# Optimization experiments

Measured on AMD Instinct MI355X. Metric: run time of the kernel, lower is better.

The kernel has to match this reference:

```python
import jax, jax.numpy as jnp
import numpy as np
import math

B, S_TOK = 2, 2046
NC = 2
S = S_TOK + NC                 # 2048 total sequence after prepending condition tokens
D, D_INNER, V = 512, 2048, 512
L, H, MAX_SEQ = 6, 8, 2048
DH = D // H
PAD = 0


def setup_inputs() -> dict:
    key = jax.random.key(0)
    ks = iter(jax.random.split(key, 48))
    def nrm(shape, scale=0.02):
        return jax.random.normal(next(ks), shape, jnp.float32) * scale
    inp = {}
    inp["x_tokens"] = jax.random.randint(next(ks), (B, S_TOK), 0, V)
    inp["conditions"] = jax.random.normal(next(ks), (B, NC), jnp.float32)
    inp["times_to_chord"] = jax.random.uniform(next(ks), (B, S_TOK), jnp.float32) * 8.0
    inp["emb"] = nrm((V, D), 0.1).at[PAD].set(0.0)  # padding_idx row zeroed
    inp["pos"] = nrm((1, MAX_SEQ, D), 0.1)
    inp["cond_W1"] = nrm((NC, 1, D // 2)); inp["cond_b1"] = jnp.zeros((NC, D // 2))
    inp["cond_W2"] = nrm((NC, D // 2, D)); inp["cond_b2"] = jnp.zeros((NC, D))
    inp["null_cond"] = nrm((NC, D), 0.1)
    inp["ttc_W"] = nrm((1, D_INNER)); inp["ttc_b"] = jnp.zeros((D_INNER,))
    for nm in ["Wq", "Wk", "Wv", "Wo"]:
        inp[nm] = nrm((L, D, D))
    for nm in ["bq", "bk", "bv", "bo"]:
        inp[nm] = jnp.zeros((L, D))
    inp["E"] = nrm((L, MAX_SEQ, DH), 1.0)  # torch.randn relative-position embedding
    inp["ffn_W1"] = nrm((L, D, D_INNER)); inp["ffn_b1"] = jnp.zeros((L, D_INNER))
    inp["ffn_W2"] = nrm((L, D_INNER, D)); inp["ffn_b2"] = jnp.zeros((L, D))
    inp["ln1_g"] = jnp.ones((L, D)); inp["ln1_b"] = jnp.zeros((L, D))
    inp["ln2_g"] = jnp.ones((L, D)); inp["ln2_b"] = jnp.zeros((L, D))
    inp["fc_W"] = nrm((D, V), 0.1); inp["fc_b"] = jnp.zeros((V,))
    return inp


def _layer_norm(x, g, b, eps=1e-6):
    mu = x.mean(-1, keepdims=True)
    var = ((x - mu) ** 2).mean(-1, keepdims=True)
    return (x - mu) / jnp.sqrt(var + eps) * g + b


def _rel_attn(x, bias, Wq, bq, Wk, bk, Wv, bv, Wo, bo, E):
    # RelativeGlobalAttention: QE masking + skewing trick (Huang et al. 2018)
    Bb, Sq, _ = x.shape
    q = (x @ Wq + bq).reshape(Bb, Sq, H, DH).transpose(0, 2, 1, 3)  # [B,H,S,dh]
    k = (x @ Wk + bk).reshape(Bb, Sq, H, DH).transpose(0, 2, 1, 3)
    v = (x @ Wv + bv).reshape(Bb, Sq, H, DH).transpose(0, 2, 1, 3)
    e = E[MAX_SEQ - Sq:]                                  # [M,dh], M == Sq here
    QE = jnp.einsum('bhld,md->bhlm', q, e)                # [B,H,S,M]
    M = QE.shape[-1]
    # row l keeps columns m >= M-1-l  (torch _qe_masking)
    qe_mask = (jnp.arange(M)[None, :] >= (M - 1 - jnp.arange(Sq))[:, None])
    QE = QE * qe_mask.astype(QE.dtype)
    # skewing: pad one column on the left, reshape, drop first row
    padded = jnp.pad(QE, ((0, 0), (0, 0), (0, 0), (1, 0)))
    Srel = padded.reshape(Bb, H, M + 1, Sq)[:, :, 1:, :]  # [B,H,S,S]
    logits = (jnp.einsum('bhld,bhmd->bhlm', q, k) + Srel) / math.sqrt(DH) + bias
    attn = jax.nn.softmax(logits, axis=-1)
    out = jnp.einsum('bhlm,bhmd->bhld', attn, v)
    out = out.transpose(0, 2, 1, 3).reshape(Bb, Sq, D)
    return out @ Wo + bo


def _forward(x_tokens, conditions, times_to_chord, emb, pos, cond_W1, cond_b1,
             cond_W2, cond_b2, null_cond, ttc_W, ttc_b, Wq, bq, Wk, bk, Wv, bv,
             Wo, bo, E, ffn_W1, ffn_b1, ffn_W2, ffn_b2, ln1_g, ln1_b, ln2_g,
             ln2_b, fc_W, fc_b):
    x = emb[x_tokens] * math.sqrt(D)                      # [B,S_tok,D]
    # generate_mask on tokens padded with -1 for the NC condition slots
    tok_pad = jnp.pad(x_tokens, ((0, 0), (NC, 0)), constant_values=-1)
    causal = jnp.triu(jnp.ones((S, S), bool), 1)          # True above diagonal
    key_pad = tok_pad == PAD                              # [B,S] pad keys
    attn_bias = jnp.where(causal[None] | key_pad[:, None, :],
                          -jnp.inf, 0.0)[:, None]         # [B,1,S,S]
    # condition MLPs with NaN -> learned null-condition substitution
    c = conditions[..., None]                             # [B,NC,1]
    nan = jnp.isnan(c)
    cm = jnp.where(nan, 0.0, c)
    h1 = jax.nn.relu(jnp.einsum('bci,cio->bco', cm, cond_W1) + cond_b1[None])
    ce = jnp.einsum('bci,cio->bco', h1, cond_W2) + cond_b2[None]   # [B,NC,D]
    ce = jnp.where(nan, null_cond[None], ce)
    x = jnp.concatenate([ce, x], axis=1)                  # [B,S,D]
    ttc = jnp.concatenate([jnp.repeat(times_to_chord[:, :1], NC, axis=1),
                           times_to_chord], axis=1)       # [B,S]
    chord = (8.0 - ttc)[..., None] @ ttc_W + ttc_b        # [B,S,D_INNER]
    x = x + pos[:, :S]
    for l in range(L):
        attn_out = _rel_attn(x, attn_bias, Wq[l], bq[l], Wk[l], bk[l],
                             Wv[l], bv[l], Wo[l], bo[l], E[l])
        out1 = _layer_norm(attn_out + x, ln1_g[l], ln1_b[l])
        ffn = jax.nn.relu(out1 @ ffn_W1[l] + ffn_b1[l]) + chord
        ffn = ffn @ ffn_W2[l] + ffn_b2[l]
        x = _layer_norm(out1 + ffn, ln2_g[l], ln2_b[l])
    return x @ fc_W + fc_b                                # [B,S,V]


def reference(x_tokens, conditions, times_to_chord, emb, pos, cond_W1, cond_b1,
              cond_W2, cond_b2, null_cond, ttc_W, ttc_b, Wq, bq, Wk, bk, Wv, bv,
              Wo, bo, E, ffn_W1, ffn_b1, ffn_W2, ffn_b2, ln1_g, ln1_b, ln2_g,
              ln2_b, fc_W, fc_b):
    return _forward(x_tokens, conditions, times_to_chord, emb, pos, cond_W1,
                    cond_b1, cond_W2, cond_b2, null_cond, ttc_W, ttc_b, Wq, bq,
                    Wk, bk, Wv, bv, Wo, bo, E, ffn_W1, ffn_b1, ffn_W2, ffn_b2,
                    ln1_g, ln1_b, ln2_g, ln2_b, fc_W, fc_b)
```

## Files before the change

kernel.cpp:

```cpp
#include <hip/hip_runtime.h>
#include <hip/hip_bf16.h>
#include <math.h>

#define BATCH  2
#define S_TOK  2046
#define NCOND  2
#define SEQ    2048
#define DMODEL 512
#define DINNER 2048
#define NHEAD  8
#define DHEAD  64
#define NLAYER 6
#define VOCAB  512
#define MROWS  (BATCH*SEQ)

#define NSLOT_G 144
#define NSLOTS  (16 * NSLOT_G)

typedef unsigned short bf16u;
typedef __attribute__((ext_vector_type(8))) short s8frag;
typedef __attribute__((ext_vector_type(4))) float f4frag;

__device__ __forceinline__ float b2f(bf16u u) {
  union { unsigned int i; float f; } v; v.i = ((unsigned int)u) << 16; return v.f;
}
__device__ __forceinline__ bf16u f2b(float f) {
  union { float f; unsigned int i; } v; v.f = f;
  unsigned int x = v.i;
  return (bf16u)((x + 0x7fffu + ((x >> 16) & 1u)) >> 16);
}
__device__ __forceinline__ unsigned int pack2(float a, float b) {
  return (unsigned int)f2b(a) | ((unsigned int)f2b(b) << 16);
}

__device__ __forceinline__ void gld16(const bf16u* g, bf16u* l) {
  __builtin_amdgcn_global_load_lds(
      (const __attribute__((address_space(1))) unsigned int*)g,
      (__attribute__((address_space(3))) unsigned int*)l,
      16, 0, 0);
}

#define DPP_ROR(dst, src, N)                                              \
  dst = __int_as_float(__builtin_amdgcn_update_dpp(                       \
      0, __float_as_int(src), 0x120 + (N), 0xF, 0xF, true))

__device__ __forceinline__ int slot_off(int it) {
  int a = it >> 2, b = it & 3;
  return it + 2 * a * (a - 1) + a * b;
}

__global__ __launch_bounds__(256) void wt_all_kernel(
    const float* __restrict__ Wq, const float* __restrict__ Wk,
    const float* __restrict__ Wv, const float* __restrict__ Wo,
    const float* __restrict__ W1, const float* __restrict__ W2,
    const float* __restrict__ fcW,
    bf16u* __restrict__ qkvT, bf16u* __restrict__ oT,
    bf16u* __restrict__ w1T, bf16u* __restrict__ w2T, bf16u* __restrict__ fcT)
{
  int bid = blockIdx.x;
  const float* src; bf16u* dst; int N, K, kt, nt;
  if (bid < 6 * 768) {
    int L = bid / 768, t = bid - L * 768;
    if (t < 256) {
      int mat = t >> 6, tt = t & 63;
      const float* s4[4] = {Wq, Wk, Wv, Wo};
      src = s4[mat] + (size_t)L * DMODEL * DMODEL;
      dst = (mat < 3) ? (qkvT + (size_t)L * 786432 + (size_t)mat * 262144)
                      : (oT + (size_t)L * 262144);
      K = DMODEL; N = DMODEL; kt = tt >> 3; nt = tt & 7;
    } else if (t < 512) {
      int tt = t - 256;
      src = W1 + (size_t)L * DMODEL * DINNER; dst = w1T + (size_t)L * 1048576;
      K = DMODEL; N = DINNER; kt = tt >> 5; nt = tt & 31;
    } else {
      int tt = t - 512;
      src = W2 + (size_t)L * DINNER * DMODEL; dst = w2T + (size_t)L * 1048576;
      K = DINNER; N = DMODEL; kt = tt >> 3; nt = tt & 7;
    }
  } else {
    int tt = bid - 6 * 768;
    src = fcW; dst = fcT;
    K = DMODEL; N = VOCAB; kt = tt >> 3; nt = tt & 7;
  }
  __shared__ bf16u Ls[64][66];
  int tid = threadIdx.x;
  int c = tid & 63, r4 = tid >> 6;
#pragma unroll
  for (int i = 0; i < 16; i++) {
    int r = i * 4 + r4;
    Ls[r][c] = f2b(src[(size_t)(kt * 64 + r) * N + nt * 64 + c]);
  }
  __syncthreads();
#pragma unroll
  for (int i = 0; i < 16; i++) {
    int rr = i * 4 + r4;
    dst[(size_t)(nt * 64 + rr) * K + kt * 64 + c] = Ls[c][rr];
  }
}

template <int RB>
__global__ __launch_bounds__(256) void mgemm(
    const bf16u* __restrict__ A, const bf16u* __restrict__ Wt,
    const float* __restrict__ b0, const float* __restrict__ b1,
    const float* __restrict__ b2, const bf16u* __restrict__ Rb,
    float* __restrict__ Cf, bf16u* __restrict__ Cb,
    int M, int N, int K, int mode,
    const float* __restrict__ ttc, const float* __restrict__ ttcW,
    const float* __restrict__ ttcb)
{
  __shared__ bf16u Ab[RB * 32][64];
  __shared__ bf16u Bb[128][64];
  const int tid = threadIdx.x;
  const int lane = tid & 63, wave = tid >> 6;
  const int quad = lane >> 4, l16 = lane & 15;
  const int wm = wave >> 1, wn = wave & 1;

  const int nwg = gridDim.x * gridDim.y;
  const int lin = blockIdx.y * gridDim.x + blockIdx.x;
  const int swz = (lin & 7) * (nwg >> 3) + (lin >> 3);
  const int bx = swz / gridDim.y, by = swz % gridDim.y;
  const int row0 = bx * (RB * 32), col0 = by * 128;

  f4frag acc[RB][4];
#pragma unroll
  for (int i = 0; i < RB; i++)
#pragma unroll
    for (int j = 0; j < 4; j++) acc[i][j] = (f4frag){0.f, 0.f, 0.f, 0.f};

  for (int k0 = 0; k0 < K; k0 += 64) {
    if (k0) __syncthreads();
#pragma unroll
    for (int i = 0; i < RB; i++) {
      int c = i * 256 + tid;
      int r = c >> 3, goct = (c & 7) ^ (r & 7);
      gld16(&A[(size_t)(row0 + r) * K + k0 + goct * 8], &Ab[0][0] + c * 8);
    }
#pragma unroll
    for (int i = 0; i < 4; i++) {
      int c = i * 256 + tid;
      int r = c >> 3, goct = (c & 7) ^ (r & 7);
      gld16(&Wt[(size_t)(col0 + r) * K + k0 + goct * 8], &Bb[0][0] + c * 8);
    }
    __syncthreads();
#pragma unroll
    for (int kk = 0; kk < 2; kk++) {
      s8frag af[RB], bfr[4];
#pragma unroll
      for (int t = 0; t < RB; t++) {
        int ar = wm * (RB * 16) + t * 16 + l16;
        int aoct = ((kk << 2) | quad) ^ (ar & 7);
        af[t] = *(const s8frag*)&Ab[ar][aoct * 8];
      }
#pragma unroll
      for (int t = 0; t < 4; t++) {
        int br = wn * 64 + t * 16 + l16;
        int boct = ((kk << 2) | quad) ^ (br & 7);
        bfr[t] = *(const s8frag*)&Bb[br][boct * 8];
      }
#pragma unroll
      for (int mt = 0; mt < RB; mt++)
#pragma unroll
        for (int nt = 0; nt < 4; nt++)
          acc[mt][nt] = __builtin_amdgcn_mfma_f32_16x16x32_bf16(
              af[mt], bfr[nt], acc[mt][nt], 0, 0, 0);
    }
  }

  if constexpr (RB == 2) {
    if (mode == 4 && col0 >= 1024) {
      __syncthreads();
      bf16u* Ls = &Bb[0][0];
#pragma unroll
      for (int mt = 0; mt < 2; mt++)
#pragma unroll
        for (int r = 0; r < 4; r++) {
          int m = wm * 32 + mt * 16 + quad * 4 + r;
#pragma unroll
          for (int nt = 0; nt < 4; nt++) {
            int n = wn * 64 + nt * 16 + l16;
            float v = acc[mt][nt][r] + b2[(col0 + n) & 511];
            Ls[n * 64 + (m ^ ((n & 7) << 3))] = f2b(v);
          }
        }
      __syncthreads();
      bf16u* vbt_g = (bf16u*)Cf;
      int bb = row0 >> 11, i0g = row0 & (SEQ - 1);
#pragma unroll
      for (int e = 0; e < 4; e++) {
        int chunk = e * 256 + tid;
        int dloc = chunk >> 3, j8 = chunk & 7;
        int nn = (col0 + dloc) & 511;
        int h = nn >> 6, dd = nn & 63;
        uint4 val = *(const uint4*)&Ls[dloc * 64 + ((j8 * 8) ^ ((dloc & 7) << 3))];
        *(uint4*)&vbt_g[((size_t)((bb * 8 + h) * DHEAD + dd)) * SEQ + i0g + j8 * 8]
            = val;
      }
      return;
    }
  }

#pragma unroll
  for (int mt = 0; mt < RB; mt++) {
#pragma unroll
    for (int r = 0; r < 4; r++) {
      int m = row0 + wm * (RB * 16) + mt * 16 + quad * 4 + r;
      float tval = 0.f;
      if (mode == 2) {
        int bb = m >> 11, s = m & (SEQ - 1);
        int sp = (s < NCOND) ? 0 : (s - NCOND);
        tval = 8.0f - ttc[bb * S_TOK + sp];
      }
#pragma unroll
      for (int nt = 0; nt < 4; nt++) {
        int n = col0 + wn * 64 + nt * 16 + l16;
        if (mode == 4) {
          int sel = n >> 9, nn = n & 511;
          float bv = (sel == 0) ? b0[nn] : b1[nn];
          Cb[(size_t)sel * MROWS * DMODEL + (size_t)m * DMODEL + nn]
              = f2b(acc[mt][nt][r] + bv);
        } else {
          float v = acc[mt][nt][r] + b0[n];
          if (mode == 1)      v += b2f(Rb[(size_t)m * N + n]);
          else if (mode == 2) v = fmaxf(v, 0.f) + tval * ttcW[n] + ttcb[n];
          if (mode == 3) Cf[(size_t)m * N + n] = v;
          else           Cb[(size_t)m * N + n] = f2b(v);
        }
      }
    }
  }
}

__global__ __launch_bounds__(256) void ln_kernel(
    const bf16u* __restrict__ X, const float* __restrict__ g,
    const float* __restrict__ bta, bf16u* __restrict__ Y)
{
  int row = blockIdx.x, tid = threadIdx.x;
  unsigned int pr = *(const unsigned int*)&X[(size_t)row * DMODEL + 2 * tid];
  float x0 = b2f((bf16u)(pr & 0xffff)), x1 = b2f((bf16u)(pr >> 16));
  __shared__ float red[8];
  int wv = tid >> 6, ln = tid & 63;
  float s = x0 + x1;
  for (int off = 32; off; off >>= 1) s += __shfl_xor(s, off);
  if (ln == 0) red[wv] = s;
  __syncthreads();
  float mu = (red[0] + red[1] + red[2] + red[3]) * (1.0f / DMODEL);
  float d0 = x0 - mu, d1 = x1 - mu;
  float vs = d0 * d0 + d1 * d1;
  for (int off = 32; off; off >>= 1) vs += __shfl_xor(vs, off);
  if (ln == 0) red[4 + wv] = vs;
  __syncthreads();
  float var = (red[4] + red[5] + red[6] + red[7]) * (1.0f / DMODEL);
  float rstd = rsqrtf(var + 1e-6f);
  float y0 = d0 * rstd * g[2 * tid]     + bta[2 * tid];
  float y1 = d1 * rstd * g[2 * tid + 1] + bta[2 * tid + 1];
  *(unsigned int*)&Y[(size_t)row * DMODEL + 2 * tid] = pack2(y0, y1);
}

__global__ __launch_bounds__(256) void tok_embed_kernel(
    const int* __restrict__ toks, const float* __restrict__ emb,
    const float* __restrict__ pos, bf16u* __restrict__ xb)
{
  int sp = blockIdx.x, b = blockIdx.y;
  int s = sp + NCOND;
  int tok = toks[b * S_TOK + sp];
  const float* er = emb + (size_t)tok * DMODEL;
  const float* pr = pos + (size_t)s * DMODEL;
  size_t ro = ((size_t)b * SEQ + s) * DMODEL;
  int d = threadIdx.x * 2;
  float v0 = er[d]     * 22.62741699796952f + pr[d];
  float v1 = er[d + 1] * 22.62741699796952f + pr[d + 1];
  *(unsigned int*)&xb[ro + d] = pack2(v0, v1);
}

__global__ __launch_bounds__(256) void cond_embed_kernel(
    const float* __restrict__ conds, const float* __restrict__ W1,
    const float* __restrict__ b1, const float* __restrict__ W2w,
    const float* __restrict__ b2, const float* __restrict__ nullc,
    const float* __restrict__ pos, bf16u* __restrict__ xb)
{
  int ci = blockIdx.x, b = blockIdx.y, tid = threadIdx.x;
  float c = conds[b * NCOND + ci];
  bool cn = isnan(c);
  float cm = cn ? 0.f : c;
  __shared__ float h1[DMODEL / 2];
  h1[tid] = fmaxf(cm * W1[ci * (DMODEL/2) + tid] + b1[ci * (DMODEL/2) + tid], 0.f);
  __syncthreads();
  for (int d = tid; d < DMODEL; d += 256) {
    float acc = b2[ci * DMODEL + d];
    for (int i = 0; i < DMODEL / 2; i++)
      acc = fmaf(h1[i], W2w[((size_t)ci * (DMODEL/2) + i) * DMODEL + d], acc);
    float ce = cn ? nullc[ci * DMODEL + d] : acc;
    xb[((size_t)b * SEQ + ci) * DMODEL + d] = f2b(ce + pos[(size_t)ci * DMODEL + d]);
  }
}

__global__ __launch_bounds__(256) void e_conv_kernel(
    const float* __restrict__ E, bf16u* __restrict__ Eb)
{
  int i = (blockIdx.x * 256 + threadIdx.x) * 4;
  float4 v = *(const float4*)&E[i];
  ushort4 o;
  o.x = f2b(v.x); o.y = f2b(v.y); o.z = f2b(v.z); o.w = f2b(v.w);
  *(ushort4*)&Eb[i] = o;
}

#define PS_SWZ(row) ((((row) >> 2) & 7) << 3)

__global__ __launch_bounds__(256) void attn_part(
    const bf16u* __restrict__ Q, const bf16u* __restrict__ K,
    const bf16u* __restrict__ Vt_g, const bf16u* __restrict__ Eb16,
    const int* __restrict__ toks, bf16u* __restrict__ pacc,
    float* __restrict__ pstat)
{
  const int d = blockIdx.x;
  const int xcd = d & 7, rank = d >> 3;
  const int g = xcd * 2 + (rank >= NSLOT_G);
  int rem = (rank >= NSLOT_G) ? rank - NSLOT_G : rank;
  int it = 31;
  for (;;) { int ch = (it >> 2) + 1; if (rem < ch) break; rem -= ch; --it; }
  const int c = rem;
  const int slot = g * NSLOT_G + slot_off(it) + c;
  const int b = g >> 3, h = g & 7;
  const int i0 = it * 64;

  __shared__ bf16u Kb[64][72];
  __shared__ bf16u Vt[64][72];
  __shared__ bf16u Ebs[128][72];
  __shared__ float padv[64];
  bf16u (*Ps)[72] = Kb;

  const int tid  = threadIdx.x;
  const int lane = tid & 63;
  const int wave = tid >> 6;
  const int quad = lane >> 4;
  const int l16  = lane & 15;

  const bf16u* qr = Q + ((size_t)(b * SEQ + i0 + wave * 16 + l16)) * DMODEL + h * DHEAD;
  s8frag q0 = *(const s8frag*)&qr[quad * 8];
  s8frag q1 = *(const s8frag*)&qr[32 + quad * 8];

  float m_run[4], l_run[4];
  f4frag acc[4];
#pragma unroll
  for (int r = 0; r < 4; r++) { m_run[r] = -1e30f; l_run[r] = 0.f; }
#pragma unroll
  for (int dt = 0; dt < 4; dt++) acc[dt] = (f4frag){0.f, 0.f, 0.f, 0.f};

  const int js0 = 4 * c;
  const int jsE = min(4 * c + 4, it + 1);
  const size_t vtbase = (size_t)(g * DHEAD) * SEQ;

  for (int js = js0; js < jsE; js++) {
    const int j0 = js * 64;
    const int m0 = 1984 - i0 + j0;
    __syncthreads();

#pragma unroll
    for (int e = 0; e < 2; e++) {
      int cc = e * 256 + tid;
      int jr = cc >> 3, doff = (cc & 7) * 8;
      *(uint4*)&Kb[jr][doff] =
          *(const uint4*)&K[((size_t)(b * SEQ + j0 + jr)) * DMODEL + h * DHEAD + doff];
    }
#pragma unroll
    for (int e = 0; e < 2; e++) {
      int cc = e * 256 + tid;
      int dr = cc >> 3, joff = (cc & 7) * 8;
      *(uint4*)&Vt[dr][joff] =
          *(const uint4*)&Vt_g[vtbase + (size_t)dr * SEQ + j0 + joff];
    }
    if (js == js0) {
#pragma unroll
      for (int e = 0; e < 4; e++) {
        int cc = e * 256 + tid;
        int er = cc >> 3, doff = (cc & 7) * 8;
        int m = m0 + er; int row = m > SEQ - 1 ? SEQ - 1 : m;
        *(uint4*)&Ebs[m & 127][doff] = *(const uint4*)&Eb16[(size_t)row * DHEAD + doff];
      }
    } else {
#pragma unroll
      for (int e = 0; e < 2; e++) {
        int cc = e * 256 + tid;
        int er = 64 + (cc >> 3), doff = (cc & 7) * 8;
        int m = m0 + er; int row = m > SEQ - 1 ? SEQ - 1 : m;
        *(uint4*)&Ebs[m & 127][doff] = *(const uint4*)&Eb16[(size_t)row * DHEAD + doff];
      }
    }
    if (tid < 64) {
      int j = j0 + tid;
      bool pad = (j >= NCOND) && (toks[b * S_TOK + j - NCOND] == 0);
      padv[tid] = pad ? -1e30f : 0.f;
    }
    __syncthreads();

    f4frag sc[4];
#pragma unroll
    for (int nt = 0; nt < 4; nt++) {
      s8frag k0 = *(const s8frag*)&Kb[nt * 16 + l16][quad * 8];
      s8frag k1 = *(const s8frag*)&Kb[nt * 16 + l16][32 + quad * 8];
      f4frag cc = (f4frag){0.f, 0.f, 0.f, 0.f};
      cc = __builtin_amdgcn_mfma_f32_16x16x32_bf16(q0, k0, cc, 0, 0, 0);
      cc = __builtin_amdgcn_mfma_f32_16x16x32_bf16(q1, k1, cc, 0, 0, 0);
      sc[nt] = cc;
    }

    f4frag qef[5];
#pragma unroll
    for (int f = 0; f < 5; f++) {
      int ct = f + 3 - wave;
      int m = m0 + ct * 16 + l16;
      const bf16u* erow = &Ebs[m & 127][0];
      s8frag e0 = *(const s8frag*)&erow[quad * 8];
      s8frag e1 = *(const s8frag*)&erow[32 + quad * 8];
      f4frag cc = (f4frag){0.f, 0.f, 0.f, 0.f};
      cc = __builtin_amdgcn_mfma_f32_16x16x32_bf16(q0, e0, cc, 0, 0, 0);
      cc = __builtin_amdgcn_mfma_f32_16x16x32_bf16(q1, e1, cc, 0, 0, 0);
      qef[f] = cc;
    }

    __syncthreads();

    float pvv[4];
#pragma unroll
    for (int nt = 0; nt < 4; nt++) pvv[nt] = padv[nt * 16 + l16];

    float s[4][4], mx[4];
#pragma unroll
    for (int r = 0; r < 4; r++) {
      int rloc = wave * 16 + quad * 4 + r;
      int ig = i0 + rloc;
      int t2 = quad * 4 + r;
      int v = 63 - 16 * wave + l16 - t2;
      int srcl = (lane & 48) | (v & 15);
      bool hiSrc = (l16 < 15 - t2);
#pragma unroll
      for (int nt = 0; nt < 4; nt++) {
        float pre = hiSrc ? qef[nt + 1][r] : qef[nt][r];
        float qe = __shfl(pre, srcl);
        int jl = nt * 16 + l16;
        float sv = (sc[nt][r] + qe) * 0.125f + pvv[nt];
        if (j0 + jl > ig) sv = -1e30f;
        s[nt][r] = sv;
      }
      float m = fmaxf(fmaxf(s[0][r], s[1][r]), fmaxf(s[2][r], s[3][r]));
      float tr;
      DPP_ROR(tr, m, 1); m = fmaxf(m, tr);
      DPP_ROR(tr, m, 2); m = fmaxf(m, tr);
      DPP_ROR(tr, m, 4); m = fmaxf(m, tr);
      DPP_ROR(tr, m, 8); m = fmaxf(m, tr);
      mx[r] = m;
    }
    float alpha[4];
#pragma unroll
    for (int r = 0; r < 4; r++) {
      float m_new = fmaxf(m_run[r], mx[r]);
      alpha[r] = __expf(m_run[r] - m_new);
      float psum = 0.f;
      int rloc = wave * 16 + quad * 4 + r;
#pragma unroll
      for (int nt = 0; nt < 4; nt++) {
        float p = __expf(s[nt][r] - m_new);
        Ps[rloc][(nt * 16 + l16) ^ PS_SWZ(rloc)] = f2b(p);
        psum += p;
      }
      float tr;
      DPP_ROR(tr, psum, 1); psum += tr;
      DPP_ROR(tr, psum, 2); psum += tr;
      DPP_ROR(tr, psum, 4); psum += tr;
      DPP_ROR(tr, psum, 8); psum += tr;
      l_run[r] = l_run[r] * alpha[r] + psum;
      m_run[r] = m_new;
    }
#pragma unroll
    for (int dt = 0; dt < 4; dt++)
#pragma unroll
      for (int r = 0; r < 4; r++) acc[dt][r] *= alpha[r];

    {
      int prow = wave * 16 + l16;
      int psw = PS_SWZ(prow);
      s8frag p0 = *(const s8frag*)&Ps[prow][(quad * 8) ^ psw];
      s8frag p1 = *(const s8frag*)&Ps[prow][(32 + quad * 8) ^ psw];
#pragma unroll
      for (int dt = 0; dt < 4; dt++) {
        s8frag v0 = *(const s8frag*)&Vt[dt * 16 + l16][quad * 8];
        s8frag v1 = *(const s8frag*)&Vt[dt * 16 + l16][32 + quad * 8];
        acc[dt] = __builtin_amdgcn_mfma_f32_16x16x32_bf16(p0, v0, acc[dt], 0, 0, 0);
        acc[dt] = __builtin_amdgcn_mfma_f32_16x16x32_bf16(p1, v1, acc[dt], 0, 0, 0);
      }
    }
  }

#pragma unroll
  for (int r = 0; r < 4; r++) {
    int rloc = wave * 16 + quad * 4 + r;
    if (l16 == 0) {
      pstat[(size_t)slot * 128 + rloc]      = m_run[r];
      pstat[(size_t)slot * 128 + 64 + rloc] = l_run[r];
    }
#pragma unroll
    for (int dt = 0; dt < 4; dt++)
      pacc[(size_t)slot * 4096 + rloc * 64 + dt * 16 + l16] = f2b(acc[dt][r]);
  }
}

__global__ __launch_bounds__(256) void attn_combine(
    const bf16u* __restrict__ pacc, const float* __restrict__ pstat,
    bf16u* __restrict__ O)
{
  int bid = blockIdx.x;
  int g = bid >> 5, it = bid & 31;
  int b = g >> 3, h = g & 7;
  int i0 = it * 64;
  int nc = (it >> 2) + 1;
  int base = g * NSLOT_G + slot_off(it);
  int tid = threadIdx.x;
  int row = tid >> 2, ql = tid & 3;

  float m_tot = -1e30f;
  float mc[8], lc[8];
#pragma unroll
  for (int c = 0; c < 8; c++) {
    if (c < nc) {
      size_t pb = (size_t)(base + c) * 128;
      mc[c] = pstat[pb + row];
      lc[c] = pstat[pb + 64 + row];
      m_tot = fmaxf(m_tot, mc[c]);
    }
  }
  float l_tot = 0.f, w[8];
#pragma unroll
  for (int c = 0; c < 8; c++) {
    if (c < nc) { w[c] = __expf(mc[c] - m_tot); l_tot += w[c] * lc[c]; }
    else w[c] = 0.f;
  }
  float inv = 1.0f / l_tot;

  float out[16];
#pragma unroll
  for (int k = 0; k < 16; k++) out[k] = 0.f;
#pragma unroll
  for (int c = 0; c < 8; c++) {
    if (c >= nc) break;
    const bf16u* pa = pacc + (size_t)(base + c) * 4096 + row * 64 + ql * 16;
#pragma unroll
    for (int k = 0; k < 16; k++) out[k] += w[c] * b2f(pa[k]);
  }
  bf16u* ob = O + ((size_t)(b * SEQ + i0 + row)) * DMODEL + h * DHEAD + ql * 16;
#pragma unroll
  for (int k = 0; k < 16; k++) ob[k] = f2b(out[k] * inv);
}

extern "C" void kernel_launch(void* const* d_in, const int* in_sizes, int n_in,
                              void* d_out, int out_size, void* d_ws, size_t ws_size,
                              hipStream_t stream) {
  const int*   toks  = (const int*)  d_in[0];
  const float* conds = (const float*)d_in[1];
  const float* ttc   = (const float*)d_in[2];
  const float* emb   = (const float*)d_in[3];
  const float* pos   = (const float*)d_in[4];
  const float* cW1   = (const float*)d_in[5];
  const float* cb1   = (const float*)d_in[6];
  const float* cW2   = (const float*)d_in[7];
  const float* cb2   = (const float*)d_in[8];
  const float* nullc = (const float*)d_in[9];
  const float* ttcW  = (const float*)d_in[10];
  const float* ttcb  = (const float*)d_in[11];
  const float* Wq    = (const float*)d_in[12];
  const float* Wk    = (const float*)d_in[13];
  const float* Wv    = (const float*)d_in[14];
  const float* Wo    = (const float*)d_in[15];
  const float* bq    = (const float*)d_in[16];
  const float* bk    = (const float*)d_in[17];
  const float* bv    = (const float*)d_in[18];
  const float* bo    = (const float*)d_in[19];
  const float* E     = (const float*)d_in[20];
  const float* fW1   = (const float*)d_in[21];
  const float* fb1   = (const float*)d_in[22];
  const float* fW2   = (const float*)d_in[23];
  const float* fb2   = (const float*)d_in[24];
  const float* ln1g  = (const float*)d_in[25];
  const float* ln1b  = (const float*)d_in[26];
  const float* ln2g  = (const float*)d_in[27];
  const float* ln2b  = (const float*)d_in[28];
  const float* fcW   = (const float*)d_in[29];
  const float* fcb   = (const float*)d_in[30];

  const size_t MB1 = 1024 * 1024;
  const size_t MD = (size_t)MROWS * DMODEL;
  char* p = (char*)d_ws;
  bf16u* xb    = (bf16u*)p; p += 4 * MB1;
  bf16u* qkvb  = (bf16u*)p; p += 12 * MB1;
  bf16u* hidb  = (bf16u*)p; p += 16 * MB1;
  float* pstat_old = (float*)p; p += 1 * MB1;
  bf16u* vbt   = (bf16u*)p; p += 4 * MB1;
  bf16u* ebf   = (bf16u*)p; p += 1536 * 1024;
  bf16u* WqkvT = (bf16u*)p; p += 9 * MB1;
  bf16u* WoT   = (bf16u*)p; p += 3 * MB1;
  bf16u* W1T   = (bf16u*)p; p += 12 * MB1;
  bf16u* W2T   = (bf16u*)p; p += 12 * MB1;
  bf16u* fcT   = (bf16u*)p; p += 512 * 1024;
  (void)pstat_old;
  bf16u* qb = qkvb;
  bf16u* kb = qkvb + MD;
  bf16u* vb = qkvb + 2 * MD;
  bf16u* out1b = kb;
  bf16u* t1b   = vb;
  bf16u* pacc  = vb;
  float* pstat = (float*)(pacc + (size_t)NSLOTS * 4096);

  cond_embed_kernel<<<dim3(NCOND, BATCH), 256, 0, stream>>>(
      conds, cW1, cb1, cW2, cb2, nullc, pos, xb);
  tok_embed_kernel<<<dim3(S_TOK, BATCH), 256, 0, stream>>>(toks, emb, pos, xb);
  wt_all_kernel<<<6 * 768 + 64, 256, 0, stream>>>(Wq, Wk, Wv, Wo, fW1, fW2, fcW,
      WqkvT, WoT, W1T, W2T, fcT);
  e_conv_kernel<<<(NLAYER * SEQ * DHEAD) / 1024, 256, 0, stream>>>(E, ebf);

  dim3 gQKV(MROWS / 64, 1536 / 128);
  dim3 gFF1(MROWS / 64, DINNER / 128);
  dim3 gN512(MROWS / 32, DMODEL / 128);

  for (int l = 0; l < NLAYER; l++) {
    mgemm<2><<<gQKV, 256, 0, stream>>>(xb, WqkvT + (size_t)l * 786432,
        bq + l * DMODEL, bk + l * DMODEL, bv + l * DMODEL, nullptr,
        (float*)vbt, qkvb, MROWS, 1536, DMODEL, 4, nullptr, nullptr, nullptr);

    attn_part<<<NSLOTS, 256, 0, stream>>>(qb, kb, vbt,
        ebf + (size_t)l * SEQ * DHEAD, toks, pacc, pstat);
    attn_combine<<<512, 256, 0, stream>>>(pacc, pstat, qb);

    mgemm<1><<<gN512, 256, 0, stream>>>(qb, WoT + (size_t)l * 262144,
        bo + l * DMODEL, nullptr, nullptr, xb,
        nullptr, t1b, MROWS, DMODEL, DMODEL, 1, nullptr, nullptr, nullptr);
    ln_kernel<<<MROWS, 256, 0, stream>>>(t1b, ln1g + l * DMODEL, ln1b + l * DMODEL,
        out1b);

    mgemm<2><<<gFF1, 256, 0, stream>>>(out1b, W1T + (size_t)l * 1048576,
        fb1 + l * DINNER, nullptr, nullptr, nullptr,
        nullptr, hidb, MROWS, DINNER, DMODEL, 2, ttc, ttcW, ttcb);
    mgemm<1><<<gN512, 256, 0, stream>>>(hidb, W2T + (size_t)l * 1048576,
        fb2 + l * DMODEL, nullptr, nullptr, out1b,
        nullptr, t1b, MROWS, DMODEL, DINNER, 1, nullptr, nullptr, nullptr);
    ln_kernel<<<MROWS, 256, 0, stream>>>(t1b, ln2g + l * DMODEL, ln2b + l * DMODEL,
        xb);
  }

  mgemm<1><<<gN512, 256, 0, stream>>>(xb, fcT,
      fcb, nullptr, nullptr, nullptr,
      (float*)d_out, nullptr, MROWS, VOCAB, DMODEL, 3, nullptr, nullptr, nullptr);
}
```

Measured before the change: 1.089 ms.

## Fuse attention split-K combine into partial kernel via atomic last-block counter

Removes the separate attn_combine launch. Each attn_part block increments a per-(head,row-tile) atomic counter after writing its partial results, and the last-arriving block merges all chunk partials and writes the output. This saves a kernel launch and reads partials while they are likely still in cache. The cost is threadfences, an atomic per block, and a serialized tail on the last block of each tile. The counters are zeroed once and reused across layers through modulo arithmetic.

New measurement: 3.114 ms. 2.86x slower.

```diff
diff --git a/kernel.cpp b/kernel.cpp
--- a/kernel.cpp
+++ b/kernel.cpp
@@ -96,6 +96,11 @@
     int rr = i * 4 + r4;
     dst[(size_t)(nt * 64 + rr) * K + kt * 64 + c] = Ls[c][rr];
   }
+}
+
+__global__ __launch_bounds__(256) void zero_cnt_kernel(int* __restrict__ c)
+{
+  c[blockIdx.x * 256 + threadIdx.x] = 0;
 }
 
 template <int RB>
@@ -310,7 +315,7 @@
     const bf16u* __restrict__ Q, const bf16u* __restrict__ K,
     const bf16u* __restrict__ Vt_g, const bf16u* __restrict__ Eb16,
     const int* __restrict__ toks, bf16u* __restrict__ pacc,
-    float* __restrict__ pstat)
+    float* __restrict__ pstat, bf16u* __restrict__ O, int* __restrict__ cnt)
 {
   const int d = blockIdx.x;
   const int xcd = d & 7, rank = d >> 3;
@@ -327,6 +332,7 @@
   __shared__ bf16u Vt[64][72];
   __shared__ bf16u Ebs[128][72];
   __shared__ float padv[64];
+  __shared__ int lastf;
   bf16u (*Ps)[72] = Kb;
 
   const int tid  = threadIdx.x;
@@ -502,53 +508,53 @@
     for (int dt = 0; dt < 4; dt++)
       pacc[(size_t)slot * 4096 + rloc * 64 + dt * 16 + l16] = f2b(acc[dt][r]);
   }
-}
-
-__global__ __launch_bounds__(256) void attn_combine(
-    const bf16u* __restrict__ pacc, const float* __restrict__ pstat,
-    bf16u* __restrict__ O)
-{
-  int bid = blockIdx.x;
-  int g = bid >> 5, it = bid & 31;
-  int b = g >> 3, h = g & 7;
-  int i0 = it * 64;
-  int nc = (it >> 2) + 1;
-  int base = g * NSLOT_G + slot_off(it);
-  int tid = threadIdx.x;
-  int row = tid >> 2, ql = tid & 3;
-
-  float m_tot = -1e30f;
-  float mc[8], lc[8];
-#pragma unroll
-  for (int c = 0; c < 8; c++) {
-    if (c < nc) {
-      size_t pb = (size_t)(base + c) * 128;
-      mc[c] = pstat[pb + row];
-      lc[c] = pstat[pb + 64 + row];
-      m_tot = fmaxf(m_tot, mc[c]);
-    }
-  }
-  float l_tot = 0.f, w[8];
-#pragma unroll
-  for (int c = 0; c < 8; c++) {
-    if (c < nc) { w[c] = __expf(mc[c] - m_tot); l_tot += w[c] * lc[c]; }
-    else w[c] = 0.f;
-  }
-  float inv = 1.0f / l_tot;
-
-  float out[16];
-#pragma unroll
-  for (int k = 0; k < 16; k++) out[k] = 0.f;
-#pragma unroll
-  for (int c = 0; c < 8; c++) {
-    if (c >= nc) break;
-    const bf16u* pa = pacc + (size_t)(base + c) * 4096 + row * 64 + ql * 16;
-#pragma unroll
-    for (int k = 0; k < 16; k++) out[k] += w[c] * b2f(pa[k]);
-  }
-  bf16u* ob = O + ((size_t)(b * SEQ + i0 + row)) * DMODEL + h * DHEAD + ql * 16;
-#pragma unroll
-  for (int k = 0; k < 16; k++) ob[k] = f2b(out[k] * inv);
+
+  const int nc = (it >> 2) + 1;
+  __threadfence();
+  if (tid == 0) {
+    int old = atomicAdd(&cnt[(g << 5) | it], 1);
+    lastf = ((old % nc) == nc - 1) ? 1 : 0;
+  }
+  __syncthreads();
+  if (!lastf) return;
+  __threadfence();
+
+  {
+    const int base = g * NSLOT_G + slot_off(it);
+    const int row = tid >> 2, ql = tid & 3;
+    float m_tot = -1e30f;
+    float mc[8], lc[8];
+#pragma unroll
+    for (int cc = 0; cc < 8; cc++) {
+      if (cc < nc) {
+        size_t pb = (size_t)(base + cc) * 128;
+        mc[cc] = pstat[pb + row];
+        lc[cc] = pstat[pb + 64 + row];
+        m_tot = fmaxf(m_tot, mc[cc]);
+      }
+    }
+    float l_tot = 0.f, w[8];
+#pragma unroll
+    for (int cc = 0; cc < 8; cc++) {
+      if (cc < nc) { w[cc] = __expf(mc[cc] - m_tot); l_tot += w[cc] * lc[cc]; }
+      else w[cc] = 0.f;
+    }
+    float inv = 1.0f / l_tot;
+
+    float out[16];
+#pragma unroll
+    for (int k = 0; k < 16; k++) out[k] = 0.f;
+#pragma unroll
+    for (int cc = 0; cc < 8; cc++) {
+      if (cc >= nc) break;
+      const bf16u* pa = pacc + (size_t)(base + cc) * 4096 + row * 64 + ql * 16;
+#pragma unroll
+      for (int k = 0; k < 16; k++) out[k] += w[cc] * b2f(pa[k]);
+    }
+    bf16u* ob = O + ((size_t)(b * SEQ + i0 + row)) * DMODEL + h * DHEAD + ql * 16;
+#pragma unroll
+    for (int k = 0; k < 16; k++) ob[k] = f2b(out[k] * inv);
+  }
 }
 
 extern "C" void kernel_launch(void* const* d_in, const int* in_sizes, int n_in,
@@ -600,6 +606,7 @@
   bf16u* W1T   = (bf16u*)p; p += 12 * MB1;
   bf16u* W2T   = (bf16u*)p; p += 12 * MB1;
   bf16u* fcT   = (bf16u*)p; p += 512 * 1024;
+  int*   cnt   = (int*)p;   p += 4096;
   (void)pstat_old;
   bf16u* qb = qkvb;
   bf16u* kb = qkvb + MD;
@@ -615,6 +622,7 @@
   wt_all_kernel<<<6 * 768 + 64, 256, 0, stream>>>(Wq, Wk, Wv, Wo, fW1, fW2, fcW,
       WqkvT, WoT, W1T, W2T, fcT);
   e_conv_kernel<<<(NLAYER * SEQ * DHEAD) / 1024, 256, 0, stream>>>(E, ebf);
+  zero_cnt_kernel<<<2, 256, 0, stream>>>(cnt);
 
   dim3 gQKV(MROWS / 64, 1536 / 128);
   dim3 gFF1(MROWS / 64, DINNER / 128);
@@ -626,8 +634,7 @@
         (float*)vbt, qkvb, MROWS, 1536, DMODEL, 4, nullptr, nullptr, nullptr);
 
     attn_part<<<NSLOTS, 256, 0, stream>>>(qb, kb, vbt,
-        ebf + (size_t)l * SEQ * DHEAD, toks, pacc, pstat);
-    attn_combine<<<512, 256, 0, stream>>>(pacc, pstat, qb);
+        ebf + (size_t)l * SEQ * DHEAD, toks, pacc, pstat, qb, cnt);
 
     mgemm<1><<<gN512, 256, 0, stream>>>(qb, WoT + (size_t)l * 262144,
         bo + l * DMODEL, nullptr, nullptr, xb,
```
